# Optimization experiments

Measured on AMD Instinct MI355X. Metric: run time of the kernel, lower is better.

Reference implementation:

```python
import jax, jax.numpy as jnp
import numpy as np

B, S, D, H, P = 4, 4096, 1024, 8, 32
K = D // H  # head_dim = 128


def setup_inputs() -> dict:
    key = jax.random.key(0)
    ks = jax.random.split(key, 12)
    f = lambda k, shape, s: jax.random.normal(k, shape, dtype=jnp.float32) * s
    return {
        "x": f(ks[0], (B, S, D), 1.0),
        "W_proj": f(ks[1], (H, K, D), 0.03),
        "resonance_freqs": f(ks[2], (H, K), 0.01),
        "pol_W": f(ks[3], (H, P, K), 0.08),
        "pol_b": jnp.zeros((H, P), jnp.float32),
        "imp_W1": f(ks[4], (16, 1), 0.5),               # Linear(1, 16)
        "imp_b1": jnp.zeros((16,), jnp.float32),
        "imp_W2": f(ks[5], (1, 16), 0.25),              # Linear(16, 1)
        "imp_b2": jnp.zeros((1,), jnp.float32),
        "out_W": f(ks[6], (D, D), 0.03),                # Linear(dim, dim)
        "out_b": jnp.zeros((D,), jnp.float32),
        "ln_g": jnp.ones((D,), jnp.float32),
        "ln_b": jnp.zeros((D,), jnp.float32),
        "causal": 1,
    }


def reference(x, W_proj, resonance_freqs, pol_W, pol_b, imp_W1, imp_b1,
              imp_W2, imp_b2, out_W, out_b, ln_g, ln_b, causal):
    Bx, Sx, Dx = x.shape
    nH = W_proj.shape[0]
    # per-head projection + resonance frequency modulation -> (B, H, S, K)
    heads = jnp.einsum('bsd,hkd->bhsk', x, W_proj)
    heads = heads * jnp.cos(resonance_freqs * jnp.pi)[None, :, None, :]

    # --- GuaXiangDuiChong: learned cross-head impedance ---
    summary = heads.mean(axis=2)                                   # (B, H, K)
    pol = jnp.tanh(jnp.einsum('bhk,hpk->bhp', summary, pol_W) + pol_b[None])
    pol = pol / jnp.maximum(jnp.linalg.norm(pol, axis=-1, keepdims=True), 1e-12)
    dots = jnp.einsum('bhp,bgp->bhg', pol, pol)                    # (B, H, H)
    z = dots[..., None]                                            # (B, H, H, 1)
    hid = jax.nn.gelu(z * imp_W1[:, 0] + imp_b1, approximate=False)  # (B, H, H, 16)
    imp = jax.nn.softplus(jnp.einsum('bijc,oc->bijo', hid, imp_W2) + imp_b2)[..., 0]
    eye = jnp.eye(nH, dtype=x.dtype)
    impedance = imp * (1.0 - eye)                                  # (B, H, H)

    # --- cross-head transfer ---
    # h_i += sum_{j != i} heads_j / (1 + imp[i,j]) * 0.1, causally mean-masked.
    coef = (0.1 / (1.0 + impedance)) * (1.0 - eye)                 # zero diagonal (i == j skipped)
    transfer = jnp.einsum('bij,bjsk->bisk', coef, heads)           # (B, H, S, K)
    if causal and Sx > 1:
        # masked_fill(t>s)+mean over t of a key-independent tensor == scale by (s+1)/S
        scale = (jnp.arange(Sx, dtype=x.dtype) + 1.0) / Sx
        transfer = transfer * scale[None, None, :, None]
    out_heads = heads + transfer

    merged = out_heads.transpose(0, 2, 1, 3).reshape(Bx, Sx, Dx)   # cat heads on last dim
    y = merged @ out_W.T + out_b + x                               # dropout is identity in eval
    mu = y.mean(-1, keepdims=True)
    var = ((y - mu) ** 2).mean(-1, keepdims=True)
    normed = (y - mu) / jnp.sqrt(var + 1e-5) * ln_g + ln_b
    return normed, impedance
```

## Files before the change

### kernel.cpp

```cpp
#include <hip/hip_runtime.h>

typedef __bf16 bf16x8 __attribute__((ext_vector_type(8)));
typedef float f32x4 __attribute__((ext_vector_type(4)));
typedef unsigned short us8 __attribute__((ext_vector_type(8)));

#define PI_F 3.14159265358979323846f

__device__ __forceinline__ unsigned short f2bf(float f) {
    unsigned u = __float_as_uint(f);
    u += 0x7FFFu + ((u >> 16) & 1u);
    return (unsigned short)(u >> 16);
}
__device__ __forceinline__ float bf2f(unsigned short h) {
    return __uint_as_float(((unsigned)h) << 16);
}

__device__ __forceinline__ void async16(const void* g, void* l) {
    __builtin_amdgcn_global_load_lds(
        (const __attribute__((address_space(1))) unsigned int*)g,
        (__attribute__((address_space(3))) unsigned int*)l, 16, 0, 0);
}

__global__ __launch_bounds__(256) void prep_k(const float* __restrict__ W,
                                              const float* __restrict__ fr,
                                              const float* __restrict__ Wo,
                                              unsigned short* __restrict__ W1b,
                                              unsigned short* __restrict__ Wob) {
    int idx = blockIdx.x * 256 + threadIdx.x;
    if (idx < (1 << 20)) {
        int n = idx >> 10, d = idx & 1023;
        int k = n >> 3, h = n & 7;
        float c = cosf(fr[h * 128 + k] * PI_F);
        W1b[idx] = f2bf(W[((h * 128 + k) << 10) + d] * c);
    } else {
        int i2 = idx - (1 << 20);
        int n = i2 >> 10, dp = i2 & 1023;
        int k = dp >> 3, h = dp & 7;
        Wob[i2] = f2bf(Wo[(n << 10) + h * 128 + k]);
    }
}

__global__ __launch_bounds__(256) void xbar_cast(const float* __restrict__ x,
                                                 unsigned short* __restrict__ xb,
                                                 float* __restrict__ part) {
    int bid = blockIdx.x;
    int b = bid >> 8;
    int s0 = (bid & 255) * 16;
    int t = threadIdx.x;
    float a0 = 0.f, a1 = 0.f, a2 = 0.f, a3 = 0.f;
    for (int i = 0; i < 16; ++i) {
        long row = (long)b * 4096 + s0 + i;
        float4 v = ((const float4*)x)[row * 256 + t];
        a0 += v.x; a1 += v.y; a2 += v.z; a3 += v.w;
        ushort4 u;
        u.x = f2bf(v.x); u.y = f2bf(v.y); u.z = f2bf(v.z); u.w = f2bf(v.w);
        ((ushort4*)xb)[row * 256 + t] = u;
    }
    float4 p; p.x = a0; p.y = a1; p.z = a2; p.w = a3;
    ((float4*)part)[bid * 256 + t] = p;
}

__global__ __launch_bounds__(256) void xbar_r(const float* __restrict__ part,
                                              float* __restrict__ xbar) {
    __shared__ float sl[256];
    int blk = blockIdx.x;
    int b = blk >> 3, dgrp = blk & 7;
    int t = threadIdx.x;
    int col = dgrp * 128 + (t & 127);
    int ih = t >> 7;
    float s = 0.f;
    for (int i = 0; i < 128; ++i) {
        int cb = b * 256 + ih * 128 + i;
        s += part[cb * 1024 + col];
    }
    sl[t] = s;
    __syncthreads();
    if (t < 128) xbar[b * 1024 + col] = sl[t] + sl[t + 128];
}

__global__ __launch_bounds__(256) void summary_k(const float* __restrict__ xbar,
                                                 const float* __restrict__ W,
                                                 const float* __restrict__ fr,
                                                 float* __restrict__ summary) {
    int wave = (blockIdx.x * 256 + threadIdx.x) >> 6;
    int lane = threadIdx.x & 63;
    int b = wave >> 10, hk = wave & 1023;
    int h = hk >> 7, k = hk & 127;
    const float* wrow = &W[(h * 128 + k) << 10];
    const float* xrow = &xbar[b << 10];
    float s = 0.f;
    for (int d = lane; d < 1024; d += 64) s += xrow[d] * wrow[d];
    for (int off = 32; off; off >>= 1) s += __shfl_down(s, off);
    if (lane == 0) {
        float c = cosf(fr[h * 128 + k] * PI_F);
        summary[wave] = s * c * (1.0f / 4096.0f);
    }
}

__global__ __launch_bounds__(256) void imp_k(const float* __restrict__ summary,
                                             const float* __restrict__ pol_W,
                                             const float* __restrict__ pol_b,
                                             const float* __restrict__ imp_W1,
                                             const float* __restrict__ imp_b1,
                                             const float* __restrict__ imp_W2,
                                             const float* __restrict__ imp_b2,
                                             float* __restrict__ coef_out,
                                             float* __restrict__ imp_out) {
    __shared__ float pol[4][8][32];
    __shared__ float rn[32];
    int t = threadIdx.x;
    for (int o = t; o < 1024; o += 256) {
        int b = o >> 8, h = (o >> 5) & 7, p = o & 31;
        const float* srow = &summary[(b * 8 + h) * 128];
        const float* wrow = &pol_W[(h * 32 + p) * 128];
        float acc = pol_b[h * 32 + p];
        for (int k = 0; k < 128; ++k) acc += srow[k] * wrow[k];
        pol[b][h][p] = tanhf(acc);
    }
    __syncthreads();
    if (t < 32) {
        int b = t >> 3, h = t & 7;
        float ss = 0.f;
        for (int p = 0; p < 32; ++p) { float v = pol[b][h][p]; ss += v * v; }
        rn[t] = 1.0f / fmaxf(sqrtf(ss), 1e-12f);
    }
    __syncthreads();
    {
        int b = t >> 6, i = (t >> 3) & 7, j = t & 7;
        float d = 0.f;
        for (int p = 0; p < 32; ++p) d += pol[b][i][p] * pol[b][j][p];
        d *= rn[b * 8 + i] * rn[b * 8 + j];
        float s = imp_b2[0];
        for (int c = 0; c < 16; ++c) {
            float z = d * imp_W1[c] + imp_b1[c];
            float gl = 0.5f * z * (1.0f + erff(z * 0.70710678118654752f));
            s += gl * imp_W2[c];
        }
        float sp = fmaxf(s, 0.0f) + log1pf(expf(-fabsf(s)));
        float impv = (i == j) ? 0.0f : sp;
        imp_out[t] = impv;
        coef_out[t] = (i == j) ? 0.0f : 0.1f / (1.0f + impv);
    }
}

#define VMCNT(n) asm volatile("s_waitcnt vmcnt(" #n ")" ::: "memory")
#define NOPW ((void)0)
#define SBAR() __builtin_amdgcn_s_barrier()

__device__ __forceinline__ void swz256(int n, long& rowBase, long& colBase) {
    int xcd = n & 7, s = n >> 3;
    rowBase = (long)(xcd * 8 + (s & 7)) * 256;
    colBase = (long)(s >> 3) * 256;
}

#define STG(sPtr, dPtr, koff, slot)                                          \
    async16((sPtr) + (koff), (dPtr) + (slot) * 16384);                       \
    async16((sPtr) + (koff) + 262144, (dPtr) + (slot) * 16384 + 8192);

#define DS_A(h, slot)                                                        \
    _Pragma("unroll") for (int i_ = 0; i_ < 4; ++i_)                         \
        af[i_] = *(const bf16x8*)(rdA + (slot) * 16384 + ((h) * 4 + i_) * 1024);

#define DS_B(slot)                                                           \
    _Pragma("unroll") for (int i_ = 0; i_ < 4; ++i_)                         \
        bf[i_] = *(const bf16x8*)(rdB + (slot) * 16384 + i_ * 1024);

#define MF(h)                                                                \
    __builtin_amdgcn_s_setprio(1);                                           \
    _Pragma("unroll") for (int i_ = 0; i_ < 4; ++i_)                         \
        _Pragma("unroll") for (int j_ = 0; j_ < 4; ++j_)                     \
            acc[(h) * 4 + i_][j_] = __builtin_amdgcn_mfma_f32_16x16x32_bf16( \
                af[i_], bf[j_], acc[(h) * 4 + i_][j_], 0, 0, 0);             \
    __builtin_amdgcn_s_setprio(0);

#define GROUP(R0, R1, S0, S1, DO_ST, KNXT, VM_MID, VM_END)                   \
    {                                                                        \
        bf16x8 af[4], bf[4];                                                 \
        DS_A(0, R0) DS_B(R0)                                                 \
        if (DO_ST) { STG(sA, stDstA, (KNXT), S0) }                           \
        SBAR(); MF(0) SBAR();                                                \
        DS_A(1, R0)                                                          \
        if (DO_ST) { STG(sB, stDstB, (KNXT), S0) }                           \
        VM_MID; SBAR(); MF(1) SBAR();                                        \
        DS_A(0, R1) DS_B(R1)                                                 \
        if (DO_ST) { STG(sA, stDstA, (KNXT) + 64, S1) }                      \
        SBAR(); MF(0) SBAR();                                                \
        DS_A(1, R1)                                                          \
        if (DO_ST) { STG(sB, stDstB, (KNXT) + 64, S1) }                      \
        VM_END; SBAR(); MF(1) SBAR();                                        \
    }

__device__ __forceinline__ void gemm8_core(const char* gAB, const char* gBB,
                                           char* smem, const int t,
                                           f32x4 acc[8][4]) {
    const int l = t & 63, wid = t >> 6;
    const int wm = wid >> 2, wn = wid & 3;
    const long stOff = (long)((wid << 4) + (t & 15)) * 2048 + ((t >> 4) & 3) * 16;
    const char* sA = gAB + stOff;
    const char* sB = gBB + stOff;
    char* As = smem;
    char* Bs = smem + 65536;
    char* stDstA = As + wid * 1024;
    char* stDstB = Bs + wid * 1024;
    const char* rdA = As + wm * 8192 + l * 16;
    const char* rdB = Bs + wn * 4096 + l * 16;

    STG(sA, stDstA, 0, 0)
    STG(sB, stDstB, 0, 0)
    STG(sA, stDstA, 64, 1)
    STG(sB, stDstB, 64, 1)
    VMCNT(4);
    SBAR();

    int kb = 128;
    for (int it = 0; it < 7; ++it) {
        GROUP(0, 1, 2, 3, true, kb, VMCNT(4), VMCNT(4))
        GROUP(2, 3, 0, 1, true, kb + 128, VMCNT(4), VMCNT(4))
        kb += 256;
    }
    GROUP(0, 1, 2, 3, true, 1920, VMCNT(4), VMCNT(4))
    GROUP(2, 3, 0, 1, false, 0, VMCNT(0), NOPW)
}

__global__ __launch_bounds__(512, 2) void gemm1_mix(
    const unsigned short* __restrict__ A, const unsigned short* __restrict__ B,
    const float* __restrict__ coef, const int* __restrict__ causal,
    unsigned short* __restrict__ C) {
    __shared__ char smem[131072];
    __shared__ float cfs[64];
    const int t = threadIdx.x;
    long rowBase, colBase;
    swz256(blockIdx.x, rowBase, colBase);
    const int b = (int)(rowBase >> 12);
    if (t < 64) cfs[t] = coef[b * 64 + t];
    const int causalv = causal[0];

    f32x4 acc[8][4] = {};
    gemm8_core((const char*)A + rowBase * 2048, (const char*)B + colBase * 2048,
               smem, t, acc);

    const int l = t & 63, wid = t >> 6;
    const int wm = wid >> 2, wn = wid & 3;
    const int q = l >> 4, c16 = l & 15;
    float* slab = (float*)smem;
#pragma unroll
    for (int p = 0; p < 8; ++p) {
        if (wm == (p >> 2)) {
            const int m0 = (p & 3) * 2;
#pragma unroll
            for (int m2 = 0; m2 < 2; ++m2)
#pragma unroll
                for (int ni = 0; ni < 4; ++ni)
#pragma unroll
                    for (int r = 0; r < 4; ++r)
                        slab[(m2 * 16 + q * 4 + r) * 264 + wn * 64 + ni * 16 + c16] =
                            acc[m0 + m2][ni][r];
        }
        __syncthreads();
#pragma unroll
        for (int gg = 0; gg < 2; ++gg) {
            const int g = t + gg * 512;
            const int row32 = g >> 5, kg = g & 31;
            const float* src = slab + row32 * 264 + kg * 8;
            float v[8];
#pragma unroll
            for (int j = 0; j < 8; ++j) v[j] = src[j];
            const long row = rowBase + p * 32 + row32;
            const float scale =
                causalv ? (float)((row & 4095) + 1) * (1.0f / 4096.0f) : 1.0f;
            us8 o;
#pragma unroll
            for (int i = 0; i < 8; ++i) {
                float ts = 0.f;
#pragma unroll
                for (int j = 0; j < 8; ++j) ts += cfs[i * 8 + j] * v[j];
                o[i] = f2bf(v[i] + scale * ts);
            }
            *(us8*)(C + row * 1024 + colBase + kg * 8) = o;
        }
        __syncthreads();
    }
}

__global__ __launch_bounds__(512, 2) void gemm_bt(const unsigned short* __restrict__ A,
                                                  const unsigned short* __restrict__ B,
                                                  unsigned short* __restrict__ C) {
    __shared__ char smem[131072];
    const int t = threadIdx.x;
    long rowBase, colBase;
    swz256(blockIdx.x, rowBase, colBase);

    f32x4 acc[8][4] = {};
    gemm8_core((const char*)A + rowBase * 2048, (const char*)B + colBase * 2048,
               smem, t, acc);

    const int l = t & 63, wid = t >> 6;
    const int wm = wid >> 2, wn = wid & 3;
    const int q = l >> 4, c16 = l & 15;
#pragma unroll
    for (int mi = 0; mi < 8; ++mi)
#pragma unroll
        for (int ni = 0; ni < 4; ++ni) {
            const long col = colBase + wn * 64 + ni * 16 + c16;
            const long row0 = rowBase + wm * 128 + mi * 16 + q * 4;
#pragma unroll
            for (int r = 0; r < 4; ++r)
                C[(row0 + r) * 1024 + col] = f2bf(acc[mi][ni][r]);
        }
}

__global__ __launch_bounds__(256) void ln_k(const unsigned short* __restrict__ ypre,
                                            const float* __restrict__ x,
                                            const float* __restrict__ outb,
                                            const float* __restrict__ gam,
                                            const float* __restrict__ bet,
                                            float* __restrict__ out) {
    int row = blockIdx.x;
    int t = threadIdx.x;
    long base = (long)row * 1024 + t * 4;
    ushort4 yp = *(const ushort4*)(ypre + base);
    float4 xv = *(const float4*)(x + base);
    float4 bv = *(const float4*)(outb + t * 4);
    float y0 = bf2f(yp.x) + xv.x + bv.x;
    float y1 = bf2f(yp.y) + xv.y + bv.y;
    float y2 = bf2f(yp.z) + xv.z + bv.z;
    float y3 = bf2f(yp.w) + xv.w + bv.w;
    float s = y0 + y1 + y2 + y3;
    float ss = y0 * y0 + y1 * y1 + y2 * y2 + y3 * y3;
    for (int off = 32; off; off >>= 1) {
        s += __shfl_down(s, off);
        ss += __shfl_down(ss, off);
    }
    __shared__ float red[8];
    int wv = t >> 6, ln = t & 63;
    if (ln == 0) { red[wv] = s; red[4 + wv] = ss; }
    __syncthreads();
    float S1 = red[0] + red[1] + red[2] + red[3];
    float S2 = red[4] + red[5] + red[6] + red[7];
    float mu = S1 * (1.0f / 1024.0f);
    float var = S2 * (1.0f / 1024.0f) - mu * mu;
    float rs = 1.0f / sqrtf(var + 1e-5f);
    float4 gv = *(const float4*)(gam + t * 4);
    float4 bb = *(const float4*)(bet + t * 4);
    float4 o;
    o.x = (y0 - mu) * rs * gv.x + bb.x;
    o.y = (y1 - mu) * rs * gv.y + bb.y;
    o.z = (y2 - mu) * rs * gv.z + bb.z;
    o.w = (y3 - mu) * rs * gv.w + bb.w;
    *(float4*)(out + base) = o;
}

extern "C" void kernel_launch(void* const* d_in, const int* in_sizes, int n_in,
                              void* d_out, int out_size, void* d_ws, size_t ws_size,
                              hipStream_t stream) {
    const float* x       = (const float*)d_in[0];
    const float* W_proj  = (const float*)d_in[1];
    const float* freqs   = (const float*)d_in[2];
    const float* pol_W   = (const float*)d_in[3];
    const float* pol_b   = (const float*)d_in[4];
    const float* imp_W1  = (const float*)d_in[5];
    const float* imp_b1  = (const float*)d_in[6];
    const float* imp_W2  = (const float*)d_in[7];
    const float* imp_b2  = (const float*)d_in[8];
    const float* out_W   = (const float*)d_in[9];
    const float* out_b   = (const float*)d_in[10];
    const float* ln_g    = (const float*)d_in[11];
    const float* ln_b    = (const float*)d_in[12];
    const int*   causal  = (const int*)d_in[13];
    float* out = (float*)d_out;

    char* ws = (char*)d_ws;
    unsigned short* xb      = (unsigned short*)(ws + 0);
    unsigned short* merged  = (unsigned short*)(ws + 33554432);
    unsigned short* w1b     = (unsigned short*)(ws + 67108864);
    unsigned short* wob     = (unsigned short*)(ws + 69206016);
    float* xbar             = (float*)(ws + 71303168);
    float* summary          = (float*)(ws + 71319552);
    float* coef             = (float*)(ws + 71335936);
    float* part             = (float*)merged;
    unsigned short* ypre    = xb;

    prep_k<<<8192, 256, 0, stream>>>(W_proj, freqs, out_W, w1b, wob);
    xbar_cast<<<1024, 256, 0, stream>>>(x, xb, part);
    xbar_r<<<32, 256, 0, stream>>>(part, xbar);
    summary_k<<<1024, 256, 0, stream>>>(xbar, W_proj, freqs, summary);
    imp_k<<<1, 256, 0, stream>>>(summary, pol_W, pol_b, imp_W1, imp_b1,
                                 imp_W2, imp_b2, coef, out + 16777216);
    gemm1_mix<<<256, 512, 0, stream>>>(xb, w1b, coef, causal, merged);
    gemm_bt<<<256, 512, 0, stream>>>(merged, wob, ypre);
    ln_k<<<16384, 256, 0, stream>>>(ypre, x, out_b, ln_g, ln_b, out);
}
```

Baseline: 298.4 us.

## Restructure GEMM main loop into single-barrier per-phase pipeline over four LDS slots

Replaces the four-barrier GROUP macro with a per-phase PH macro that issues the global-to-LDS prefetch two slots ahead, waits with a deeper vmcnt, and uses a single barrier before reading LDS and running both MFMA halves. The goal is fewer s_barrier stalls and more loads in flight per k-step. Because the loop no longer ends on a barrier, a __syncthreads is added before the epilogue reuses shared memory. The risk is a race on slot reuse, since there is only one barrier between a slot being read and the same slot being overwritten by a later prefetch.

```diff
diff --git a/kernel.cpp b/kernel.cpp
--- a/kernel.cpp
+++ b/kernel.cpp
@@ -144,7 +144,6 @@
 }
 
 #define VMCNT(n) asm volatile("s_waitcnt vmcnt(" #n ")" ::: "memory")
-#define NOPW ((void)0)
 #define SBAR() __builtin_amdgcn_s_barrier()
 
 __device__ __forceinline__ void swz256(int n, long& rowBase, long& colBase) {
@@ -157,37 +156,35 @@
     async16((sPtr) + (koff), (dPtr) + (slot) * 16384);                       \
     async16((sPtr) + (koff) + 262144, (dPtr) + (slot) * 16384 + 8192);
 
-#define DS_A(h, slot)                                                        \
-    _Pragma("unroll") for (int i_ = 0; i_ < 4; ++i_)                         \
-        af[i_] = *(const bf16x8*)(rdA + (slot) * 16384 + ((h) * 4 + i_) * 1024);
-
-#define DS_B(slot)                                                           \
-    _Pragma("unroll") for (int i_ = 0; i_ < 4; ++i_)                         \
-        bf[i_] = *(const bf16x8*)(rdB + (slot) * 16384 + i_ * 1024);
-
-#define MF(h)                                                                \
-    __builtin_amdgcn_s_setprio(1);                                           \
-    _Pragma("unroll") for (int i_ = 0; i_ < 4; ++i_)                         \
-        _Pragma("unroll") for (int j_ = 0; j_ < 4; ++j_)                     \
-            acc[(h) * 4 + i_][j_] = __builtin_amdgcn_mfma_f32_16x16x32_bf16( \
-                af[i_], bf[j_], acc[(h) * 4 + i_][j_], 0, 0, 0);             \
-    __builtin_amdgcn_s_setprio(0);
-
-#define GROUP(R0, R1, S0, S1, DO_ST, KNXT, VM_MID, VM_END)                   \
+#define PH(p, DO_ST, KOFF, VM)                                               \
     {                                                                        \
-        bf16x8 af[4], bf[4];                                                 \
-        DS_A(0, R0) DS_B(R0)                                                 \
-        if (DO_ST) { STG(sA, stDstA, (KNXT), S0) }                           \
-        SBAR(); MF(0) SBAR();                                                \
-        DS_A(1, R0)                                                          \
-        if (DO_ST) { STG(sB, stDstB, (KNXT), S0) }                           \
-        VM_MID; SBAR(); MF(1) SBAR();                                        \
-        DS_A(0, R1) DS_B(R1)                                                 \
-        if (DO_ST) { STG(sA, stDstA, (KNXT) + 64, S1) }                      \
-        SBAR(); MF(0) SBAR();                                                \
-        DS_A(1, R1)                                                          \
-        if (DO_ST) { STG(sB, stDstB, (KNXT) + 64, S1) }                      \
-        VM_END; SBAR(); MF(1) SBAR();                                        \
+        if (DO_ST) {                                                         \
+            STG(sA, stDstA, (KOFF), ((p) + 2) & 3)                           \
+            STG(sB, stDstB, (KOFF), ((p) + 2) & 3)                           \
+        }                                                                    \
+        VM;                                                                  \
+        SBAR();                                                              \
+        const char* pA = rdA + ((p) & 3) * 16384;                            \
+        const char* pB = rdB + ((p) & 3) * 16384;                            \
+        bf16x8 af[4], bv[4];                                                 \
+        _Pragma("unroll") for (int i_ = 0; i_ < 4; ++i_)                     \
+            af[i_] = *(const bf16x8*)(pA + i_ * 1024);                       \
+        _Pragma("unroll") for (int i_ = 0; i_ < 4; ++i_)                     \
+            bv[i_] = *(const bf16x8*)(pB + i_ * 1024);                       \
+        __builtin_amdgcn_s_setprio(1);                                       \
+        _Pragma("unroll") for (int mi = 0; mi < 4; ++mi)                     \
+            _Pragma("unroll") for (int ni = 0; ni < 4; ++ni)                 \
+                acc[mi][ni] = __builtin_amdgcn_mfma_f32_16x16x32_bf16(       \
+                    af[mi], bv[ni], acc[mi][ni], 0, 0, 0);                   \
+        __builtin_amdgcn_s_setprio(0);                                       \
+        _Pragma("unroll") for (int i_ = 0; i_ < 4; ++i_)                     \
+            af[i_] = *(const bf16x8*)(pA + (4 + i_) * 1024);                 \
+        __builtin_amdgcn_s_setprio(1);                                       \
+        _Pragma("unroll") for (int mi = 0; mi < 4; ++mi)                     \
+            _Pragma("unroll") for (int ni = 0; ni < 4; ++ni)                 \
+                acc[4 + mi][ni] = __builtin_amdgcn_mfma_f32_16x16x32_bf16(   \
+                    af[mi], bv[ni], acc[4 + mi][ni], 0, 0, 0);               \
+        __builtin_amdgcn_s_setprio(0);                                       \
     }
 
 __device__ __forceinline__ void gemm8_core(const char* gAB, const char* gBB,
@@ -209,17 +206,19 @@
     STG(sB, stDstB, 0, 0)
     STG(sA, stDstA, 64, 1)
     STG(sB, stDstB, 64, 1)
-    VMCNT(4);
-    SBAR();
 
     int kb = 128;
-    for (int it = 0; it < 7; ++it) {
-        GROUP(0, 1, 2, 3, true, kb, VMCNT(4), VMCNT(4))
-        GROUP(2, 3, 0, 1, true, kb + 128, VMCNT(4), VMCNT(4))
+    for (int grp = 0; grp < 7; ++grp) {
+        PH(0, true, kb, VMCNT(8))
+        PH(1, true, kb + 64, VMCNT(8))
+        PH(2, true, kb + 128, VMCNT(8))
+        PH(3, true, kb + 192, VMCNT(8))
         kb += 256;
     }
-    GROUP(0, 1, 2, 3, true, 1920, VMCNT(4), VMCNT(4))
-    GROUP(2, 3, 0, 1, false, 0, VMCNT(0), NOPW)
+    PH(0, true, 1920, VMCNT(8))
+    PH(1, true, 1984, VMCNT(8))
+    PH(2, false, 0, VMCNT(4))
+    PH(3, false, 0, VMCNT(0))
 }
 
 __global__ __launch_bounds__(512, 2) void gemm1_mix(
@@ -238,6 +237,7 @@
     f32x4 acc[8][4] = {};
     gemm8_core((const char*)A + rowBase * 2048, (const char*)B + colBase * 2048,
                smem, t, acc);
+    __syncthreads();
 
     const int l = t & 63, wid = t >> 6;
     const int wm = wid >> 2, wn = wid & 3;
```

Result: no change. 295.8 us (-0.9%).

## Restructure GEMM mainloop to double-buffered 128-wide K stages with new LDS layout

Applied to the files above, without the earlier changes.

Replaces the four-slot 64-wide K pipeline with a two-buffer scheme that stages 128 K columns per step (A and B halves in a ping-pong 64 KB buffer each), changes the LDS staging/read layout and the vmcnt waits, and uses an asm barrier with memory clobber. The aim is to cut barrier and wait overhead per K step and improve how global-to-LDS loads overlap with MFMA work. A syncthreads is added before the epilogue reuses shared memory. It risks LDS bank conflicts from the new layout and less prefetch depth.

```diff
diff --git a/kernel.cpp b/kernel.cpp
--- a/kernel.cpp
+++ b/kernel.cpp
@@ -144,8 +144,7 @@
 }
 
 #define VMCNT(n) asm volatile("s_waitcnt vmcnt(" #n ")" ::: "memory")
-#define NOPW ((void)0)
-#define SBAR() __builtin_amdgcn_s_barrier()
+#define ABAR() asm volatile("s_barrier" ::: "memory")
 
 __device__ __forceinline__ void swz256(int n, long& rowBase, long& colBase) {
     int xcd = n & 7, s = n >> 3;
@@ -153,73 +152,75 @@
     colBase = (long)(s >> 3) * 256;
 }
 
-#define STG(sPtr, dPtr, koff, slot)                                          \
-    async16((sPtr) + (koff), (dPtr) + (slot) * 16384);                       \
-    async16((sPtr) + (koff) + 262144, (dPtr) + (slot) * 16384 + 8192);
-
-#define DS_A(h, slot)                                                        \
+#define STAGE(gsrc, ldst, h, ko)                                             \
+    async16((gsrc) + (h) * 262144 + (ko), (ldst) + (h) * 16384);             \
+    async16((gsrc) + (h) * 262144 + 131072 + (ko), (ldst) + (h) * 16384 + 8192);
+
+#define RD_A(base, mi0, ks)                                                  \
     _Pragma("unroll") for (int i_ = 0; i_ < 4; ++i_)                         \
-        af[i_] = *(const bf16x8*)(rdA + (slot) * 16384 + ((h) * 4 + i_) * 1024);
-
-#define DS_B(slot)                                                           \
+        af[i_] = *(const bf16x8*)((base) + ((mi0) + i_) * 2048 + (ks) * 1024);
+
+#define RD_B(base, ks)                                                       \
     _Pragma("unroll") for (int i_ = 0; i_ < 4; ++i_)                         \
-        bf[i_] = *(const bf16x8*)(rdB + (slot) * 16384 + i_ * 1024);
-
-#define MF(h)                                                                \
+        bv[i_] = *(const bf16x8*)((base) + i_ * 2048 + (ks) * 1024);
+
+#define MFMA16(m0)                                                           \
     __builtin_amdgcn_s_setprio(1);                                           \
-    _Pragma("unroll") for (int i_ = 0; i_ < 4; ++i_)                         \
-        _Pragma("unroll") for (int j_ = 0; j_ < 4; ++j_)                     \
-            acc[(h) * 4 + i_][j_] = __builtin_amdgcn_mfma_f32_16x16x32_bf16( \
-                af[i_], bf[j_], acc[(h) * 4 + i_][j_], 0, 0, 0);             \
+    _Pragma("unroll") for (int mi = 0; mi < 4; ++mi)                         \
+        _Pragma("unroll") for (int ni = 0; ni < 4; ++ni)                     \
+            acc[(m0) + mi][ni] = __builtin_amdgcn_mfma_f32_16x16x32_bf16(    \
+                af[mi], bv[ni], acc[(m0) + mi][ni], 0, 0, 0);                \
     __builtin_amdgcn_s_setprio(0);
 
-#define GROUP(R0, R1, S0, S1, DO_ST, KNXT, VM_MID, VM_END)                   \
+#define GRP(RB, DO_ST, KO, VMW)                                              \
     {                                                                        \
-        bf16x8 af[4], bf[4];                                                 \
-        DS_A(0, R0) DS_B(R0)                                                 \
-        if (DO_ST) { STG(sA, stDstA, (KNXT), S0) }                           \
-        SBAR(); MF(0) SBAR();                                                \
-        DS_A(1, R0)                                                          \
-        if (DO_ST) { STG(sB, stDstB, (KNXT), S0) }                           \
-        VM_MID; SBAR(); MF(1) SBAR();                                        \
-        DS_A(0, R1) DS_B(R1)                                                 \
-        if (DO_ST) { STG(sA, stDstA, (KNXT) + 64, S1) }                      \
-        SBAR(); MF(0) SBAR();                                                \
-        DS_A(1, R1)                                                          \
-        if (DO_ST) { STG(sB, stDstB, (KNXT) + 64, S1) }                      \
-        VM_END; SBAR(); MF(1) SBAR();                                        \
-    }
-
-__device__ __forceinline__ void gemm8_core(const char* gAB, const char* gBB,
-                                           char* smem, const int t,
-                                           f32x4 acc[8][4]) {
+        char* Ad = smem + ((RB) ^ 1) * 65536 + t * 16;                       \
+        char* Bd = Ad + 32768;                                               \
+        const char* Ar = smem + (RB) * 65536 + wm * 16384 + qoff;            \
+        const char* Br = smem + (RB) * 65536 + 32768 + wn * 8192 + qoff;     \
+        bf16x8 af[4], bv[4];                                                 \
+                                                                    \
+        if (DO_ST) { STAGE(sA, Ad, 0, KO) }                                  \
+        VMCNT(VMW); ABAR();                                                  \
+        RD_A(Ar, 0, 0) RD_B(Br, 0)                                           \
+        MFMA16(0) ABAR();                                                    \
+                                                                    \
+        RD_A(Ar, 4, 0)                                                       \
+        if (DO_ST) { STAGE(sA, Ad, 1, KO) }                                  \
+        ABAR(); MFMA16(4) ABAR();                                            \
+                                                                    \
+        RD_A(Ar, 0, 1) RD_B(Br, 1)                                           \
+        if (DO_ST) { STAGE(sB, Bd, 0, KO) }                                  \
+        ABAR(); MFMA16(0) ABAR();                                            \
+                                                                    \
+        RD_A(Ar, 4, 1)                                                       \
+        if (DO_ST) { STAGE(sB, Bd, 1, KO) }                                  \
+        ABAR(); MFMA16(4) ABAR();                                            \
+    }
+
+__device__ __forceinline__ void gemm256_core(const char* gAB, const char* gBB,
+                                             char* smem, const int t,
+                                             f32x4 acc[8][4]) {
     const int l = t & 63, wid = t >> 6;
     const int wm = wid >> 2, wn = wid & 3;
-    const long stOff = (long)((wid << 4) + (t & 15)) * 2048 + ((t >> 4) & 3) * 16;
-    const char* sA = gAB + stOff;
-    const char* sB = gBB + stOff;
-    char* As = smem;
-    char* Bs = smem + 65536;
-    char* stDstA = As + wid * 1024;
-    char* stDstB = Bs + wid * 1024;
-    const char* rdA = As + wm * 8192 + l * 16;
-    const char* rdB = Bs + wn * 4096 + l * 16;
-
-    STG(sA, stDstA, 0, 0)
-    STG(sB, stDstB, 0, 0)
-    STG(sA, stDstA, 64, 1)
-    STG(sB, stDstB, 64, 1)
-    VMCNT(4);
-    SBAR();
-
-    int kb = 128;
-    for (int it = 0; it < 7; ++it) {
-        GROUP(0, 1, 2, 3, true, kb, VMCNT(4), VMCNT(4))
-        GROUP(2, 3, 0, 1, true, kb + 128, VMCNT(4), VMCNT(4))
-        kb += 256;
-    }
-    GROUP(0, 1, 2, 3, true, 1920, VMCNT(4), VMCNT(4))
-    GROUP(2, 3, 0, 1, false, 0, VMCNT(0), NOPW)
+    const long rowPart =
+        (long)(((t >> 7) << 4) + (t & 15)) * 2048 + ((t >> 4) & 7) * 16;
+    const char* sA = gAB + rowPart;
+    const char* sB = gBB + rowPart;
+    const int qoff = ((l >> 4) << 8) + (l & 15) * 16;
+
+    {
+        char* Ad = smem + t * 16;
+        char* Bd = Ad + 32768;
+        STAGE(sA, Ad, 0, 0) STAGE(sA, Ad, 1, 0)
+        STAGE(sB, Bd, 0, 0) STAGE(sB, Bd, 1, 0)
+    }
+    for (int it = 0; it < 15; ++it) {
+        const int RB = it & 1;
+        const long KO = (long)(it + 1) * 128;
+        GRP(RB, true, KO, 2)
+    }
+    GRP(1, false, 0, 0)
 }
 
 __global__ __launch_bounds__(512, 2) void gemm1_mix(
@@ -236,8 +237,9 @@
     const int causalv = causal[0];
 
     f32x4 acc[8][4] = {};
-    gemm8_core((const char*)A + rowBase * 2048, (const char*)B + colBase * 2048,
-               smem, t, acc);
+    gemm256_core((const char*)A + rowBase * 2048, (const char*)B + colBase * 2048,
+                 smem, t, acc);
+    __syncthreads();
 
     const int l = t & 63, wid = t >> 6;
     const int wm = wid >> 2, wn = wid & 3;
@@ -291,8 +293,8 @@
     swz256(blockIdx.x, rowBase, colBase);
 
     f32x4 acc[8][4] = {};
-    gemm8_core((const char*)A + rowBase * 2048, (const char*)B + colBase * 2048,
-               smem, t, acc);
+    gemm256_core((const char*)A + rowBase * 2048, (const char*)B + colBase * 2048,
+                 smem, t, acc);
 
     const int l = t & 63, wid = t >> 6;
     const int wm = wid >> 2, wn = wid & 3;
```

New measurement: 305.3 us. 2.3% more time.
